# Kernel tuning notes

Measured on AMD Instinct MI355X. Metric: run time of the kernel, lower is better.

The kernel has to match this reference:

```python
import jax, jax.numpy as jnp
import numpy as np

DIM = 1024
HEADS = 16
HEAD_DIM = DIM // HEADS
DECAY = 0.95
EPS = 1e-5


def setup_inputs() -> dict:
    key = jax.random.key(0)
    ks = jax.random.split(key, 11)
    B, S, D = 2, 2048, DIM
    s = 1.0 / np.sqrt(D)
    inp = {
        'x': jax.random.normal(ks[0], (B, S, D), dtype=jnp.float32),
        'Wq': jax.random.normal(ks[1], (D, D), dtype=jnp.float32) * s,
        'bq': jnp.zeros((D,), jnp.float32),
        'Wk': jax.random.normal(ks[2], (D, D), dtype=jnp.float32) * s,
        'bk': jnp.zeros((D,), jnp.float32),
        'Wv': jax.random.normal(ks[3], (D, D), dtype=jnp.float32) * s,
        'bv': jnp.zeros((D,), jnp.float32),
        'Wo': jax.random.normal(ks[4], (D, D), dtype=jnp.float32) * s,
        'bo': jnp.zeros((D,), jnp.float32),
        'gamma': jnp.ones((D,), jnp.float32),
        'beta': jnp.zeros((D,), jnp.float32),
    }
    return inp


def _decay_mask(S, dtype):
    idx = jnp.arange(S)
    diff = (idx[:, None] - idx[None, :]).astype(jnp.float32)
    # decay^(i-j) for i >= j, else 0
    mask = jnp.where(diff >= 0, jnp.exp(diff * np.log(DECAY)), 0.0)
    return mask.astype(dtype)


def reference(x, Wq, bq, Wk, bk, Wv, bv, Wo, bo, gamma, beta):
    B, S, D = x.shape
    H, hd = HEADS, HEAD_DIM

    def split_heads(y):  # [B,S,D] -> [B,H,S,hd]
        return y.reshape(B, S, H, hd).transpose(0, 2, 1, 3)

    q = split_heads(x @ Wq + bq)
    k = split_heads(x @ Wk + bk)
    v = split_heads(x @ Wv + bv)

    mask = _decay_mask(S, x.dtype)  # [S,S]
    scores = jnp.einsum('bhid,bhjd->bhij', q, k) * mask
    out = jnp.einsum('bhij,bhjd->bhid', scores, v)  # [B,H,S,hd]

    out = out.transpose(0, 2, 1, 3).reshape(B, S, D)
    out = out @ Wo + bo

    # GroupNorm(H groups) applied over channel dim with seq as spatial dim
    y = out.transpose(0, 2, 1)            # [B,D,S]
    yg = y.reshape(B, H, hd, S)
    mu = yg.mean(axis=(2, 3), keepdims=True)
    var = yg.var(axis=(2, 3), keepdims=True)
    yn = (yg - mu) / jnp.sqrt(var + EPS)
    yn = yn.reshape(B, D, S) * gamma[None, :, None] + beta[None, :, None]
    return yn.transpose(0, 2, 1)          # [B,S,D]
```

## Files before the change

### kernel.cpp

```cpp
#include <hip/hip_runtime.h>
#include <hip/hip_bf16.h>

typedef unsigned short u16;
typedef __attribute__((ext_vector_type(8))) short short8;
typedef __attribute__((ext_vector_type(4))) float f32x4;
typedef __attribute__((ext_vector_type(4))) unsigned short u16x4;

#define SEQ 2048
#define NH 16
#define HD 64
#define DM 1024
#define LN_DECAY (-0.051293294387550536f)
#define WIN_TILES 4

__device__ __forceinline__ float b2f(u16 u) {
    return __uint_as_float(((unsigned int)u) << 16);
}
__device__ __forceinline__ u16 f2b(float f) {
    unsigned int u = __float_as_uint(f);
    u += 0x7fffu + ((u >> 16) & 1u);
    return (u16)(u >> 16);
}
__device__ __forceinline__ f32x4 mfma16(short8 a, short8 b, f32x4 c) {
    return __builtin_amdgcn_mfma_f32_16x16x32_bf16(a, b, c, 0, 0, 0);
}
__device__ __forceinline__ void gld_lds16(const u16* g, u16* l) {
    __builtin_amdgcn_global_load_lds(
        (const __attribute__((address_space(1))) void*)g,
        (__attribute__((address_space(3))) void*)l, 16, 0, 0);
}
__device__ __forceinline__ int detect_fl(const u16* Wq, int lane) {
    int hit = 0;
#pragma unroll
    for (int j = 0; j < 4; j++) {
        u16 u = Wq[2*(lane + 64*j)];
        if (((u >> 7) & 0xFF) >= 0xC0) hit = 1;
    }
    return (__ballot(hit) != 0ULL) ? 1 : 0;
}

__global__ __launch_bounds__(256) void prep(
    const void* __restrict__ x,
    const void* __restrict__ Wq, const void* __restrict__ Wk,
    const void* __restrict__ Wv, const void* __restrict__ Wo,
    const void* __restrict__ bq, const void* __restrict__ bk,
    const void* __restrict__ bv, const void* __restrict__ bo,
    const void* __restrict__ gamma, const void* __restrict__ beta,
    u16* __restrict__ xc,
    u16* __restrict__ WqT, u16* __restrict__ WkT,
    u16* __restrict__ WvT, u16* __restrict__ WoT,
    u16* __restrict__ bqc, u16* __restrict__ bkc, u16* __restrict__ bvc,
    u16* __restrict__ boc, u16* __restrict__ gammac, u16* __restrict__ betac,
    int* __restrict__ flag, float* __restrict__ statsAcc)
{
    __shared__ u16 tileS[32][33];
    int bid = blockIdx.x, tid = threadIdx.x;
    int fl = detect_fl((const u16*)Wq, tid & 63);

    if (bid < 4096) {
        int i = (bid*256 + tid)*4;
        if (fl) {
            f32x4 v = *(const f32x4*)((const float*)x + i);
            u16x4 o = { f2b(v[0]), f2b(v[1]), f2b(v[2]), f2b(v[3]) };
            *(u16x4*)(xc + i) = o;
        } else {
            *(u16x4*)(xc + i) = *(const u16x4*)((const u16*)x + i);
        }
    } else if (bid == 4096) {
        const void* ins[6] = {bq, bk, bv, bo, gamma, beta};
        u16* outs[6] = {bqc, bkc, bvc, boc, gammac, betac};
        int i = tid*4;
#pragma unroll
        for (int a = 0; a < 6; a++) {
            if (fl) {
                f32x4 v = *(const f32x4*)((const float*)ins[a] + i);
                u16x4 o = { f2b(v[0]), f2b(v[1]), f2b(v[2]), f2b(v[3]) };
                *(u16x4*)(outs[a] + i) = o;
            } else {
                *(u16x4*)(outs[a] + i) = *(const u16x4*)((const u16*)ins[a] + i);
            }
        }
        if (tid == 0) *flag = fl;
        if (tid < 64) statsAcc[tid] = 0.f;
    } else {
        int tb = bid - 4097;
        int wsel = tb >> 10, tile = tb & 1023;
        const void* W = (wsel==0) ? Wq : (wsel==1) ? Wk : (wsel==2) ? Wv : Wo;
        u16* T        = (wsel==0) ? WqT : (wsel==1) ? WkT : (wsel==2) ? WvT : WoT;
        int bn = (tile & 31)*32, bk_ = (tile >> 5)*32;
        int r = tid >> 5, c = tid & 31;
#pragma unroll
        for (int i2 = 0; i2 < 4; i2++) {
            size_t idx = (size_t)(bk_ + r + i2*8)*DM + bn + c;
            tileS[r + i2*8][c] = fl ? f2b(((const float*)W)[idx]) : ((const u16*)W)[idx];
        }
        __syncthreads();
#pragma unroll
        for (int i2 = 0; i2 < 4; i2++)
            T[(size_t)(bn + r + i2*8)*DM + bk_ + c] = tileS[c][r + i2*8];
    }
}

__device__ __forceinline__ void gemm_core(
    const u16* __restrict__ A, const u16* __restrict__ BT,
    u16* As, u16* Bs, int m0, int n0, int t, f32x4 (&acc)[4][4])
{
    int l = t & 63;
    int lane16 = l & 15, quad = l >> 4;
    int w = t >> 6;
    int wm = (w >> 1) * 64, wn = (w & 1) * 64;

    int srow   = t >> 2;
    int schunk = (t & 3) ^ ((t >> 3) & 3);

    f32x4 zero = {0.f, 0.f, 0.f, 0.f};
#pragma unroll
    for (int i = 0; i < 4; i++)
#pragma unroll
        for (int j = 0; j < 4; j++)
            acc[i][j] = zero;

    const u16* a0 = A  + (size_t)(m0 + srow)      * DM + schunk*8;
    const u16* a1 = A  + (size_t)(m0 + srow + 64) * DM + schunk*8;
    const u16* b0 = BT + (size_t)(n0 + srow)      * DM + schunk*8;
    const u16* b1 = BT + (size_t)(n0 + srow + 64) * DM + schunk*8;

    for (int k0 = 0; k0 < DM; k0 += 32) {
        __syncthreads();
        gld_lds16(a0 + k0, &As[t*8]);
        gld_lds16(a1 + k0, &As[2048 + t*8]);
        gld_lds16(b0 + k0, &Bs[t*8]);
        gld_lds16(b1 + k0, &Bs[2048 + t*8]);
        __syncthreads();
        short8 af[4], bf[4];
#pragma unroll
        for (int i = 0; i < 4; i++) {
            int ra = wm + i*16 + lane16;
            int rb = wn + i*16 + lane16;
            af[i] = *(const short8*)(&As[ra*32 + ((quad ^ ((ra>>1)&3))*8)]);
            bf[i] = *(const short8*)(&Bs[rb*32 + ((quad ^ ((rb>>1)&3))*8)]);
        }
#pragma unroll
        for (int i = 0; i < 4; i++)
#pragma unroll
            for (int j = 0; j < 4; j++)
                acc[i][j] = mfma16(af[i], bf[j], acc[i][j]);
    }
}

__global__ __launch_bounds__(256) void gemm_qkv(
    const u16* __restrict__ x,
    const u16* __restrict__ WqT, const u16* __restrict__ WkT, const u16* __restrict__ WvT,
    const u16* __restrict__ bq, const u16* __restrict__ bk, const u16* __restrict__ bv,
    u16* __restrict__ qb, u16* __restrict__ kb, u16* __restrict__ vTb)
{
    __shared__ u16 As[128*32];
    __shared__ u16 Bs[128*32];
    int z = blockIdx.z;
    const u16* BT   = (z==0) ? WqT : (z==1) ? WkT : WvT;
    const u16* bias = (z==0) ? bq  : (z==1) ? bk  : bv;
    u16* outB       = (z==0) ? qb  : (z==1) ? kb  : vTb;
    int m0 = blockIdx.x * 128, n0 = blockIdx.y * 128, t = threadIdx.x;

    f32x4 acc[4][4];
    gemm_core(x, BT, As, Bs, m0, n0, t, acc);

    int l = t & 63, lane16 = l & 15, quad = l >> 4, w = t >> 6;
    int wm = (w >> 1) * 64, wn = (w & 1) * 64;
#pragma unroll
    for (int i = 0; i < 4; i++) {
#pragma unroll
        for (int j = 0; j < 4; j++) {
            int n = n0 + wn + j*16 + lane16;
            float bvv = b2f(bias[n]);
#pragma unroll
            for (int r = 0; r < 4; r++) {
                int m = m0 + wm + i*16 + quad*4 + r;
                float v = acc[i][j][r] + bvv;
                int b = m >> 11, sq = m & (SEQ-1);
                int h = n >> 6,  d = n & (HD-1);
                if (z == 2)
                    outB[(((size_t)(b*NH + h))*HD + d)*SEQ + sq] = f2b(v);
                else
                    outB[(((size_t)(b*NH + h))*SEQ + sq)*HD + d] = f2b(v);
            }
        }
    }
}

__global__ __launch_bounds__(256) void retention(
    const u16* __restrict__ q, const u16* __restrict__ k,
    const u16* __restrict__ vT, u16* __restrict__ attn)
{
    __shared__ u16 Ks[64*64];
    __shared__ u16 Vs[64*64];
    __shared__ u16 Ps[4][16*64];

    int qt = blockIdx.x, bh = blockIdx.y;
    int t = threadIdx.x, w = t >> 6, l = t & 63;
    int c = l & 15, qd = l >> 4;
    int qbase = qt * 64;
    int iwave = qbase + w*16;

    const u16* qh = q  + (size_t)bh * SEQ * HD;
    const u16* kh = k  + (size_t)bh * SEQ * HD;
    const u16* vh = vT + (size_t)bh * HD * SEQ;

    float D[4], E[4];
#pragma unroll
    for (int r = 0; r < 4; r++)
        D[r] = __expf((float)(qd*4 + r) * LN_DECAY);
#pragma unroll
    for (int st = 0; st < 4; st++)
        E[st] = __expf(-(float)(st*16 + c) * LN_DECAY);

    int sr = t >> 3, sc8 = t & 7;

    short8 qf[2];
#pragma unroll
    for (int kk = 0; kk < 2; kk++)
        qf[kk] = *(const short8*)(qh + (size_t)(iwave + c)*HD + kk*32 + qd*8);

    f32x4 zero = {0.f, 0.f, 0.f, 0.f};
    f32x4 oacc[4] = {zero, zero, zero, zero};

    int jt0 = (qt > WIN_TILES) ? (qt - WIN_TILES) : 0;
#pragma unroll 1
    for (int jt = jt0; jt <= qt; jt++) {
        int jbase = jt * 64;
        __syncthreads();
        {
            int r0 = sr, r1 = sr + 32;
            *(short8*)(&Ks[r0*64 + ((sc8 ^ (r0&7))*8)]) = *(const short8*)(kh + (size_t)(jbase+r0)*HD + sc8*8);
            *(short8*)(&Ks[r1*64 + ((sc8 ^ (r1&7))*8)]) = *(const short8*)(kh + (size_t)(jbase+r1)*HD + sc8*8);
            *(short8*)(&Vs[r0*64 + ((sc8 ^ (r0&7))*8)]) = *(const short8*)(vh + (size_t)r0*SEQ + jbase + sc8*8);
            *(short8*)(&Vs[r1*64 + ((sc8 ^ (r1&7))*8)]) = *(const short8*)(vh + (size_t)(r1)*SEQ + jbase + sc8*8);
        }
        __syncthreads();

        f32x4 sacc[4] = {zero, zero, zero, zero};
#pragma unroll
        for (int kk = 0; kk < 2; kk++) {
#pragma unroll
            for (int st = 0; st < 4; st++) {
                int row = st*16 + c;
                short8 bf = *(const short8*)(&Ks[row*64 + (((kk*4+qd) ^ (row&7))*8)]);
                sacc[st] = mfma16(qf[kk], bf, sacc[st]);
            }
        }

        float base = __expf((float)(iwave - jbase) * LN_DECAY);
#pragma unroll
        for (int st = 0; st < 4; st++) {
            int j = jbase + st*16 + c;
            float bE = base * E[st];
#pragma unroll
            for (int r = 0; r < 4; r++) {
                int i = iwave + qd*4 + r;
                float val = (i >= j) ? sacc[st][r] * (bE * D[r]) : 0.0f;
                int row = qd*4 + r;
                int col = st*16 + c;
                Ps[w][row*64 + (((col>>3) ^ (row&7))*8) + (col&7)] = f2b(val);
            }
        }
        asm volatile("s_waitcnt lgkmcnt(0)" ::: "memory");
        short8 pf[2];
#pragma unroll
        for (int kk = 0; kk < 2; kk++)
            pf[kk] = *(const short8*)(&Ps[w][c*64 + (((kk*4+qd) ^ (c&7))*8)]);

#pragma unroll
        for (int kk = 0; kk < 2; kk++) {
#pragma unroll
            for (int nt = 0; nt < 4; nt++) {
                int row = nt*16 + c;
                short8 vf = *(const short8*)(&Vs[row*64 + (((kk*4+qd) ^ (row&7))*8)]);
                oacc[nt] = mfma16(pf[kk], vf, oacc[nt]);
            }
        }
    }

    int b = bh >> 4, h = bh & (NH-1);
#pragma unroll
    for (int nt = 0; nt < 4; nt++) {
        int d = h*HD + nt*16 + c;
#pragma unroll
        for (int r = 0; r < 4; r++) {
            int s = iwave + qd*4 + r;
            attn[((size_t)(b*SEQ + s))*DM + d] = f2b(oacc[nt][r]);
        }
    }
}

__global__ __launch_bounds__(256) void gemm_out(
    const u16* __restrict__ attn, const u16* __restrict__ WoT,
    const u16* __restrict__ bo, float* __restrict__ proj,
    float* __restrict__ statsAcc)
{
    __shared__ u16 As[128*32];
    __shared__ u16 Bs[64*32];
    int m0 = blockIdx.x * 128, n0 = blockIdx.y * 64, t = threadIdx.x;
    int l = t & 63, lane16 = l & 15, quad = l >> 4, w = t >> 6;
    int wm = w * 32;

    int srow   = t >> 2;
    int schunk = (t & 3) ^ ((t >> 3) & 3);

    f32x4 zero = {0.f, 0.f, 0.f, 0.f};
    f32x4 acc[2][4];
#pragma unroll
    for (int i = 0; i < 2; i++)
#pragma unroll
        for (int j = 0; j < 4; j++)
            acc[i][j] = zero;

    const u16* a0 = attn + (size_t)(m0 + srow)      * DM + schunk*8;
    const u16* a1 = attn + (size_t)(m0 + srow + 64) * DM + schunk*8;
    const u16* b0 = WoT  + (size_t)(n0 + srow)      * DM + schunk*8;

    for (int k0 = 0; k0 < DM; k0 += 32) {
        __syncthreads();
        gld_lds16(a0 + k0, &As[t*8]);
        gld_lds16(a1 + k0, &As[2048 + t*8]);
        gld_lds16(b0 + k0, &Bs[t*8]);
        __syncthreads();
        short8 af[2], bf[4];
#pragma unroll
        for (int i = 0; i < 2; i++) {
            int ra = wm + i*16 + lane16;
            af[i] = *(const short8*)(&As[ra*32 + ((quad ^ ((ra>>1)&3))*8)]);
        }
#pragma unroll
        for (int j = 0; j < 4; j++) {
            int rb = j*16 + lane16;
            bf[j] = *(const short8*)(&Bs[rb*32 + ((quad ^ ((rb>>1)&3))*8)]);
        }
#pragma unroll
        for (int i = 0; i < 2; i++)
#pragma unroll
            for (int j = 0; j < 4; j++)
                acc[i][j] = mfma16(af[i], bf[j], acc[i][j]);
    }

    float s = 0.f, ss = 0.f;
#pragma unroll
    for (int j = 0; j < 4; j++) {
        int n = n0 + j*16 + lane16;
        float bvv = b2f(bo[n]);
#pragma unroll
        for (int i = 0; i < 2; i++) {
#pragma unroll
            for (int r = 0; r < 4; r++) {
                int m = m0 + wm + i*16 + quad*4 + r;
                float v = acc[i][j][r] + bvv;
                proj[(size_t)m*DM + n] = v;
                s += v; ss += v*v;
            }
        }
    }
#pragma unroll
    for (int off = 32; off > 0; off >>= 1) {
        s  += __shfl_down(s, off);
        ss += __shfl_down(ss, off);
    }
    if (l == 0) {
        int b = m0 >> 11;
        int g = n0 >> 6;
        atomicAdd(&statsAcc[(b*NH + g)*2],     s);
        atomicAdd(&statsAcc[(b*NH + g)*2 + 1], ss);
    }
}

__global__ __launch_bounds__(256) void gn_apply(
    const float* __restrict__ proj, const float* __restrict__ statsAcc,
    const u16* __restrict__ gamma, const u16* __restrict__ beta,
    const int* __restrict__ flag, void* __restrict__ outv)
{
    int base = (blockIdx.x*256 + threadIdx.x)*4;
    int d = base & (DM-1);
    int b = base >> 21;
    int g = d >> 6;
    float S  = statsAcc[(b*NH + g)*2];
    float SS = statsAcc[(b*NH + g)*2 + 1];
    const float inv = 1.0f/(float)(SEQ*HD);
    float mu = S*inv;
    float rstd = rsqrtf(SS*inv - mu*mu + 1e-5f);
    f32x4 v = *(const f32x4*)(proj + base);
    float o0 = (v[0]-mu)*rstd*b2f(gamma[d])   + b2f(beta[d]);
    float o1 = (v[1]-mu)*rstd*b2f(gamma[d+1]) + b2f(beta[d+1]);
    float o2 = (v[2]-mu)*rstd*b2f(gamma[d+2]) + b2f(beta[d+2]);
    float o3 = (v[3]-mu)*rstd*b2f(gamma[d+3]) + b2f(beta[d+3]);
    if (*flag) {
        f32x4 ov = {o0, o1, o2, o3};
        *(f32x4*)((float*)outv + base) = ov;
    } else {
        u16x4 ov = {f2b(o0), f2b(o1), f2b(o2), f2b(o3)};
        *(u16x4*)((u16*)outv + base) = ov;
    }
}

extern "C" void kernel_launch(void* const* d_in, const int* in_sizes, int n_in,
                              void* d_out, int out_size, void* d_ws, size_t ws_size,
                              hipStream_t stream) {
    const void* x     = d_in[0];
    const void* Wq    = d_in[1];
    const void* bq    = d_in[2];
    const void* Wk    = d_in[3];
    const void* bk    = d_in[4];
    const void* Wv    = d_in[5];
    const void* bv    = d_in[6];
    const void* Wo    = d_in[7];
    const void* bo    = d_in[8];
    const void* gamma = d_in[9];
    const void* beta  = d_in[10];

    const size_t MB = 1024*1024;
    char* ws = (char*)d_ws;
    int*   flag     = (int*)ws;
    u16*   bqc      = (u16*)(ws + 4096);
    u16*   bkc      = (u16*)(ws + 8192);
    u16*   bvc      = (u16*)(ws + 12288);
    u16*   boc      = (u16*)(ws + 16384);
    u16*   gammac   = (u16*)(ws + 20480);
    u16*   betac    = (u16*)(ws + 24576);
    float* statsAcc = (float*)(ws + 28672);
    u16*   xc     = (u16*)(ws + 1*MB);
    u16*   WqT    = (u16*)(ws + 9*MB);
    u16*   WkT    = (u16*)(ws + 11*MB);
    u16*   WvT    = (u16*)(ws + 13*MB);
    u16*   WoT    = (u16*)(ws + 15*MB);
    u16*   qb     = (u16*)(ws + 17*MB);
    u16*   kb     = (u16*)(ws + 25*MB);
    u16*   vTb    = (u16*)(ws + 33*MB);
    u16*   attn   = (u16*)(ws + 41*MB);
    float* proj   = (float*)(ws + 17*MB);

    prep<<<8193, 256, 0, stream>>>(x, Wq, Wk, Wv, Wo, bq, bk, bv, bo, gamma, beta,
                                   xc, WqT, WkT, WvT, WoT,
                                   bqc, bkc, bvc, boc, gammac, betac,
                                   flag, statsAcc);
    gemm_qkv<<<dim3(32, 8, 3), 256, 0, stream>>>(xc, WqT, WkT, WvT, bqc, bkc, bvc, qb, kb, vTb);
    retention<<<dim3(32, 32), 256, 0, stream>>>(qb, kb, vTb, attn);
    gemm_out<<<dim3(32, 16), 256, 0, stream>>>(attn, WoT, boc, proj, statsAcc);
    gn_apply<<<4096, 256, 0, stream>>>(proj, statsAcc, gammac, betac, flag, d_out);
}
```

Measured before the change: 201.6 us.

## Double-buffer LDS in output projection GEMM and enlarge tile to 128x128

```diff
diff --git a/kernel.cpp b/kernel.cpp
--- a/kernel.cpp
+++ b/kernel.cpp
@@ -292,24 +292,42 @@
     }
 }
 
+__device__ __forceinline__ void gout_step(
+    const u16* As, const u16* Bs, int wm, int wn, int lane16, int quad,
+    f32x4 (&acc)[4][4])
+{
+    short8 af[4], bf[4];
+#pragma unroll
+    for (int i = 0; i < 4; i++) {
+        int ra = wm + i*16 + lane16;
+        int rb = wn + i*16 + lane16;
+        af[i] = *(const short8*)(&As[ra*32 + ((quad ^ ((ra>>1)&3))*8)]);
+        bf[i] = *(const short8*)(&Bs[rb*32 + ((quad ^ ((rb>>1)&3))*8)]);
+    }
+#pragma unroll
+    for (int i = 0; i < 4; i++)
+#pragma unroll
+        for (int j = 0; j < 4; j++)
+            acc[i][j] = mfma16(af[i], bf[j], acc[i][j]);
+}
+
 __global__ __launch_bounds__(256) void gemm_out(
     const u16* __restrict__ attn, const u16* __restrict__ WoT,
     const u16* __restrict__ bo, float* __restrict__ proj,
     float* __restrict__ statsAcc)
 {
-    __shared__ u16 As[128*32];
-    __shared__ u16 Bs[64*32];
-    int m0 = blockIdx.x * 128, n0 = blockIdx.y * 64, t = threadIdx.x;
+    __shared__ u16 As0[128*32], Bs0[128*32];
+    __shared__ u16 As1[128*32], Bs1[128*32];
+    int m0 = blockIdx.x * 128, n0 = blockIdx.y * 128, t = threadIdx.x;
     int l = t & 63, lane16 = l & 15, quad = l >> 4, w = t >> 6;
-    int wm = w * 32;
-
+    int wm = (w >> 1) * 64, wn = (w & 1) * 64;
     int srow   = t >> 2;
     int schunk = (t & 3) ^ ((t >> 3) & 3);
 
     f32x4 zero = {0.f, 0.f, 0.f, 0.f};
-    f32x4 acc[2][4];
-#pragma unroll
-    for (int i = 0; i < 2; i++)
+    f32x4 acc[4][4];
+#pragma unroll
+    for (int i = 0; i < 4; i++)
 #pragma unroll
         for (int j = 0; j < 4; j++)
             acc[i][j] = zero;
@@ -317,38 +335,40 @@
     const u16* a0 = attn + (size_t)(m0 + srow)      * DM + schunk*8;
     const u16* a1 = attn + (size_t)(m0 + srow + 64) * DM + schunk*8;
     const u16* b0 = WoT  + (size_t)(n0 + srow)      * DM + schunk*8;
-
-    for (int k0 = 0; k0 < DM; k0 += 32) {
-        __syncthreads();
-        gld_lds16(a0 + k0, &As[t*8]);
-        gld_lds16(a1 + k0, &As[2048 + t*8]);
-        gld_lds16(b0 + k0, &Bs[t*8]);
-        __syncthreads();
-        short8 af[2], bf[4];
-#pragma unroll
-        for (int i = 0; i < 2; i++) {
-            int ra = wm + i*16 + lane16;
-            af[i] = *(const short8*)(&As[ra*32 + ((quad ^ ((ra>>1)&3))*8)]);
-        }
+    const u16* b1 = WoT  + (size_t)(n0 + srow + 64) * DM + schunk*8;
+
+    gld_lds16(a0, &As0[t*8]);
+    gld_lds16(a1, &As0[2048 + t*8]);
+    gld_lds16(b0, &Bs0[t*8]);
+    gld_lds16(b1, &Bs0[2048 + t*8]);
+    __syncthreads();
+
+#pragma unroll 1
+    for (int k0 = 0; k0 < DM; k0 += 64) {
+        gld_lds16(a0 + k0 + 32, &As1[t*8]);
+        gld_lds16(a1 + k0 + 32, &As1[2048 + t*8]);
+        gld_lds16(b0 + k0 + 32, &Bs1[t*8]);
+        gld_lds16(b1 + k0 + 32, &Bs1[2048 + t*8]);
+        gout_step(As0, Bs0, wm, wn, lane16, quad, acc);
+        __syncthreads();
+
+        if (k0 + 64 < DM) {
+            gld_lds16(a0 + k0 + 64, &As0[t*8]);
+            gld_lds16(a1 + k0 + 64, &As0[2048 + t*8]);
+            gld_lds16(b0 + k0 + 64, &Bs0[t*8]);
+            gld_lds16(b1 + k0 + 64, &Bs0[2048 + t*8]);
+        }
+        gout_step(As1, Bs1, wm, wn, lane16, quad, acc);
+        __syncthreads();
+    }
+
+    float s = 0.f, ss = 0.f;
+#pragma unroll
+    for (int i = 0; i < 4; i++) {
 #pragma unroll
         for (int j = 0; j < 4; j++) {
-            int rb = j*16 + lane16;
-            bf[j] = *(const short8*)(&Bs[rb*32 + ((quad ^ ((rb>>1)&3))*8)]);
-        }
-#pragma unroll
-        for (int i = 0; i < 2; i++)
-#pragma unroll
-            for (int j = 0; j < 4; j++)
-                acc[i][j] = mfma16(af[i], bf[j], acc[i][j]);
-    }
-
-    float s = 0.f, ss = 0.f;
-#pragma unroll
-    for (int j = 0; j < 4; j++) {
-        int n = n0 + j*16 + lane16;
-        float bvv = b2f(bo[n]);
-#pragma unroll
-        for (int i = 0; i < 2; i++) {
+            int n = n0 + wn + j*16 + lane16;
+            float bvv = b2f(bo[n]);
 #pragma unroll
             for (int r = 0; r < 4; r++) {
                 int m = m0 + wm + i*16 + quad*4 + r;
@@ -365,7 +385,7 @@
     }
     if (l == 0) {
         int b = m0 >> 11;
-        int g = n0 >> 6;
+        int g = (n0 + wn) >> 6;
         atomicAdd(&statsAcc[(b*NH + g)*2],     s);
         atomicAdd(&statsAcc[(b*NH + g)*2 + 1], ss);
     }
@@ -441,6 +461,6 @@
                                    flag, statsAcc);
     gemm_qkv<<<dim3(32, 8, 3), 256, 0, stream>>>(xc, WqT, WkT, WvT, bqc, bkc, bvc, qb, kb, vTb);
     retention<<<dim3(32, 32), 256, 0, stream>>>(qb, kb, vTb, attn);
-    gemm_out<<<dim3(32, 16), 256, 0, stream>>>(attn, WoT, boc, proj, statsAcc);
+    gemm_out<<<dim3(32, 8), 256, 0, stream>>>(attn, WoT, boc, proj, statsAcc);
     gn_apply<<<4096, 256, 0, stream>>>(proj, statsAcc, gammac, betac, flag, d_out);
 }
```

Result: faster. 188.9 us (-6.3%).

## Double-buffer LDS in output GEMM and enlarge tile to 128x128 with 8 waves

Applied to the files above, without the earlier changes.

```diff
diff --git a/kernel.cpp b/kernel.cpp
--- a/kernel.cpp
+++ b/kernel.cpp
@@ -292,17 +292,38 @@
     }
 }
 
-__global__ __launch_bounds__(256) void gemm_out(
+__device__ __forceinline__ void gout_step8(
+    const u16* As, const u16* Bs, int wm, int wn, int lane16, int quad,
+    f32x4 (&acc)[2][4])
+{
+    short8 af[2], bf[4];
+#pragma unroll
+    for (int i = 0; i < 2; i++) {
+        int ra = wm + i*16 + lane16;
+        af[i] = *(const short8*)(&As[ra*32 + ((quad ^ ((ra>>1)&3))*8)]);
+    }
+#pragma unroll
+    for (int j = 0; j < 4; j++) {
+        int rb = wn + j*16 + lane16;
+        bf[j] = *(const short8*)(&Bs[rb*32 + ((quad ^ ((rb>>1)&3))*8)]);
+    }
+#pragma unroll
+    for (int i = 0; i < 2; i++)
+#pragma unroll
+        for (int j = 0; j < 4; j++)
+            acc[i][j] = mfma16(af[i], bf[j], acc[i][j]);
+}
+
+__global__ __launch_bounds__(512) void gemm_out(
     const u16* __restrict__ attn, const u16* __restrict__ WoT,
     const u16* __restrict__ bo, float* __restrict__ proj,
     float* __restrict__ statsAcc)
 {
-    __shared__ u16 As[128*32];
-    __shared__ u16 Bs[64*32];
-    int m0 = blockIdx.x * 128, n0 = blockIdx.y * 64, t = threadIdx.x;
+    __shared__ u16 As0[128*32], Bs0[128*32];
+    __shared__ u16 As1[128*32], Bs1[128*32];
+    int m0 = blockIdx.x * 128, n0 = blockIdx.y * 128, t = threadIdx.x;
     int l = t & 63, lane16 = l & 15, quad = l >> 4, w = t >> 6;
-    int wm = w * 32;
-
+    int wm = (w >> 1) * 32, wn = (w & 1) * 64;
     int srow   = t >> 2;
     int schunk = (t & 3) ^ ((t >> 3) & 3);
 
@@ -314,41 +335,35 @@
         for (int j = 0; j < 4; j++)
             acc[i][j] = zero;
 
-    const u16* a0 = attn + (size_t)(m0 + srow)      * DM + schunk*8;
-    const u16* a1 = attn + (size_t)(m0 + srow + 64) * DM + schunk*8;
-    const u16* b0 = WoT  + (size_t)(n0 + srow)      * DM + schunk*8;
-
-    for (int k0 = 0; k0 < DM; k0 += 32) {
-        __syncthreads();
-        gld_lds16(a0 + k0, &As[t*8]);
-        gld_lds16(a1 + k0, &As[2048 + t*8]);
-        gld_lds16(b0 + k0, &Bs[t*8]);
-        __syncthreads();
-        short8 af[2], bf[4];
-#pragma unroll
-        for (int i = 0; i < 2; i++) {
-            int ra = wm + i*16 + lane16;
-            af[i] = *(const short8*)(&As[ra*32 + ((quad ^ ((ra>>1)&3))*8)]);
-        }
+    const u16* a = attn + (size_t)(m0 + srow) * DM + schunk*8;
+    const u16* b = WoT  + (size_t)(n0 + srow) * DM + schunk*8;
+
+    gld_lds16(a, &As0[t*8]);
+    gld_lds16(b, &Bs0[t*8]);
+    __syncthreads();
+
+#pragma unroll 1
+    for (int k0 = 0; k0 < DM; k0 += 64) {
+        gld_lds16(a + k0 + 32, &As1[t*8]);
+        gld_lds16(b + k0 + 32, &Bs1[t*8]);
+        gout_step8(As0, Bs0, wm, wn, lane16, quad, acc);
+        __syncthreads();
+
+        if (k0 + 64 < DM) {
+            gld_lds16(a + k0 + 64, &As0[t*8]);
+            gld_lds16(b + k0 + 64, &Bs0[t*8]);
+        }
+        gout_step8(As1, Bs1, wm, wn, lane16, quad, acc);
+        __syncthreads();
+    }
+
+    float s = 0.f, ss = 0.f;
+#pragma unroll
+    for (int i = 0; i < 2; i++) {
 #pragma unroll
         for (int j = 0; j < 4; j++) {
-            int rb = j*16 + lane16;
-            bf[j] = *(const short8*)(&Bs[rb*32 + ((quad ^ ((rb>>1)&3))*8)]);
-        }
-#pragma unroll
-        for (int i = 0; i < 2; i++)
-#pragma unroll
-            for (int j = 0; j < 4; j++)
-                acc[i][j] = mfma16(af[i], bf[j], acc[i][j]);
-    }
-
-    float s = 0.f, ss = 0.f;
-#pragma unroll
-    for (int j = 0; j < 4; j++) {
-        int n = n0 + j*16 + lane16;
-        float bvv = b2f(bo[n]);
-#pragma unroll
-        for (int i = 0; i < 2; i++) {
+            int n = n0 + wn + j*16 + lane16;
+            float bvv = b2f(bo[n]);
 #pragma unroll
             for (int r = 0; r < 4; r++) {
                 int m = m0 + wm + i*16 + quad*4 + r;
@@ -364,10 +379,10 @@
         ss += __shfl_down(ss, off);
     }
     if (l == 0) {
-        int b = m0 >> 11;
-        int g = n0 >> 6;
-        atomicAdd(&statsAcc[(b*NH + g)*2],     s);
-        atomicAdd(&statsAcc[(b*NH + g)*2 + 1], ss);
+        int b_ = m0 >> 11;
+        int g  = (n0 + wn) >> 6;
+        atomicAdd(&statsAcc[(b_*NH + g)*2],     s);
+        atomicAdd(&statsAcc[(b_*NH + g)*2 + 1], ss);
     }
 }
 
@@ -441,6 +456,6 @@
                                    flag, statsAcc);
     gemm_qkv<<<dim3(32, 8, 3), 256, 0, stream>>>(xc, WqT, WkT, WvT, bqc, bkc, bvc, qb, kb, vTb);
     retention<<<dim3(32, 32), 256, 0, stream>>>(qb, kb, vTb, attn);
-    gemm_out<<<dim3(32, 16), 256, 0, stream>>>(attn, WoT, boc, proj, statsAcc);
+    gemm_out<<<dim3(32, 8), 512, 0, stream>>>(attn, WoT, boc, proj, statsAcc);
     gn_apply<<<4096, 256, 0, stream>>>(proj, statsAcc, gammac, betac, flag, d_out);
 }
```

New measurement: 198.1 us. About the same (-1.7%).

## Remap blocks across XCDs, stage V-transpose stores in LDS, enlarge output GEMM tiles

Applied to the files above, without the earlier changes.

```diff
diff --git a/kernel.cpp b/kernel.cpp
--- a/kernel.cpp
+++ b/kernel.cpp
@@ -156,33 +156,72 @@
 {
     __shared__ u16 As[128*32];
     __shared__ u16 Bs[128*32];
-    int z = blockIdx.z;
+    __shared__ u16 rep[64*130];
+
+    int lin = blockIdx.x + 32*(blockIdx.y + 8*blockIdx.z);
+    int xcd = lin & 7, slot = lin >> 3;
+    int mx  = xcd*4 + (slot & 3);
+    int col = slot >> 2;
+    int ny  = col & 7, z = col >> 3;
+
     const u16* BT   = (z==0) ? WqT : (z==1) ? WkT : WvT;
     const u16* bias = (z==0) ? bq  : (z==1) ? bk  : bv;
     u16* outB       = (z==0) ? qb  : (z==1) ? kb  : vTb;
-    int m0 = blockIdx.x * 128, n0 = blockIdx.y * 128, t = threadIdx.x;
+    int m0 = mx * 128, n0 = ny * 128, t = threadIdx.x;
 
     f32x4 acc[4][4];
     gemm_core(x, BT, As, Bs, m0, n0, t, acc);
 
     int l = t & 63, lane16 = l & 15, quad = l >> 4, w = t >> 6;
     int wm = (w >> 1) * 64, wn = (w & 1) * 64;
-#pragma unroll
-    for (int i = 0; i < 4; i++) {
-#pragma unroll
-        for (int j = 0; j < 4; j++) {
-            int n = n0 + wn + j*16 + lane16;
-            float bvv = b2f(bias[n]);
-#pragma unroll
-            for (int r = 0; r < 4; r++) {
-                int m = m0 + wm + i*16 + quad*4 + r;
-                float v = acc[i][j][r] + bvv;
-                int b = m >> 11, sq = m & (SEQ-1);
-                int h = n >> 6,  d = n & (HD-1);
-                if (z == 2)
-                    outB[(((size_t)(b*NH + h))*HD + d)*SEQ + sq] = f2b(v);
-                else
-                    outB[(((size_t)(b*NH + h))*SEQ + sq)*HD + d] = f2b(v);
+
+    if (z == 2) {
+        int b = m0 >> 11, sq0 = m0 & (SEQ-1);
+#pragma unroll 1
+        for (int h = 0; h < 2; h++) {
+            if ((w & 1) == h) {
+#pragma unroll
+                for (int j = 0; j < 4; j++) {
+                    int dl = j*16 + lane16;
+                    float bvv = b2f(bias[n0 + h*64 + dl]);
+#pragma unroll
+                    for (int i = 0; i < 2; i++) {
+#pragma unroll
+                        for (int r = 0; r < 4; r++) {
+                            rep[dl*130 + wm + i*16 + quad*4 + r] =
+                                f2b(acc[i][j][r] + bvv);
+                            rep[dl*130 + wm + (i+2)*16 + quad*4 + r] =
+                                f2b(acc[i+2][j][r] + bvv);
+                        }
+                    }
+                }
+            }
+            __syncthreads();
+            int head = (n0 + h*64) >> 6;
+            int row = t >> 2, c0 = (t & 3)*32;
+            u16* dst = outB + (((size_t)(b*NH + head))*HD + row)*SEQ + sq0 + c0;
+#pragma unroll
+            for (int cc = 0; cc < 32; cc += 8) {
+                short8 v = *(const short8*)(&rep[row*130 + c0 + cc]);
+                *(short8*)(dst + cc) = v;
+            }
+            __syncthreads();
+        }
+    } else {
+#pragma unroll
+        for (int i = 0; i < 4; i++) {
+#pragma unroll
+            for (int j = 0; j < 4; j++) {
+                int n = n0 + wn + j*16 + lane16;
+                float bvv = b2f(bias[n]);
+#pragma unroll
+                for (int r = 0; r < 4; r++) {
+                    int m = m0 + wm + i*16 + quad*4 + r;
+                    float v = acc[i][j][r] + bvv;
+                    int b = m >> 11, sq = m & (SEQ-1);
+                    int hh = n >> 6, d = n & (HD-1);
+                    outB[(((size_t)(b*NH + hh))*SEQ + sq)*HD + d] = f2b(v);
+                }
             }
         }
     }
@@ -196,7 +235,11 @@
     __shared__ u16 Vs[64*64];
     __shared__ u16 Ps[4][16*64];
 
-    int qt = blockIdx.x, bh = blockIdx.y;
+    int lin = blockIdx.x + 32*blockIdx.y;
+    int xcd = lin & 7, slot = lin >> 3;
+    int bh  = xcd*4 + (slot >> 5);
+    int qt  = slot & 31;
+
     int t = threadIdx.x, w = t >> 6, l = t & 63;
     int c = l & 15, qd = l >> 4;
     int qbase = qt * 64;
@@ -298,57 +341,25 @@
     float* __restrict__ statsAcc)
 {
     __shared__ u16 As[128*32];
-    __shared__ u16 Bs[64*32];
-    int m0 = blockIdx.x * 128, n0 = blockIdx.y * 64, t = threadIdx.x;
+    __shared__ u16 Bs[128*32];
+    int lin = blockIdx.x + 32*blockIdx.y;
+    int xcd = lin & 7, slot = lin >> 3;
+    int mx  = xcd*4 + (slot & 3);
+    int ny  = slot >> 2;
+    int m0 = mx * 128, n0 = ny * 128, t = threadIdx.x;
+
+    f32x4 acc[4][4];
+    gemm_core(attn, WoT, As, Bs, m0, n0, t, acc);
+
     int l = t & 63, lane16 = l & 15, quad = l >> 4, w = t >> 6;
-    int wm = w * 32;
-
-    int srow   = t >> 2;
-    int schunk = (t & 3) ^ ((t >> 3) & 3);
-
-    f32x4 zero = {0.f, 0.f, 0.f, 0.f};
-    f32x4 acc[2][4];
-#pragma unroll
-    for (int i = 0; i < 2; i++)
-#pragma unroll
-        for (int j = 0; j < 4; j++)
-            acc[i][j] = zero;
-
-    const u16* a0 = attn + (size_t)(m0 + srow)      * DM + schunk*8;
-    const u16* a1 = attn + (size_t)(m0 + srow + 64) * DM + schunk*8;
-    const u16* b0 = WoT  + (size_t)(n0 + srow)      * DM + schunk*8;
-
-    for (int k0 = 0; k0 < DM; k0 += 32) {
-        __syncthreads();
-        gld_lds16(a0 + k0, &As[t*8]);
-        gld_lds16(a1 + k0, &As[2048 + t*8]);
-        gld_lds16(b0 + k0, &Bs[t*8]);
-        __syncthreads();
-        short8 af[2], bf[4];
-#pragma unroll
-        for (int i = 0; i < 2; i++) {
-            int ra = wm + i*16 + lane16;
-            af[i] = *(const short8*)(&As[ra*32 + ((quad ^ ((ra>>1)&3))*8)]);
-        }
+    int wm = (w >> 1) * 64, wn = (w & 1) * 64;
+    float s = 0.f, ss = 0.f;
+#pragma unroll
+    for (int i = 0; i < 4; i++) {
 #pragma unroll
         for (int j = 0; j < 4; j++) {
-            int rb = j*16 + lane16;
-            bf[j] = *(const short8*)(&Bs[rb*32 + ((quad ^ ((rb>>1)&3))*8)]);
-        }
-#pragma unroll
-        for (int i = 0; i < 2; i++)
-#pragma unroll
-            for (int j = 0; j < 4; j++)
-                acc[i][j] = mfma16(af[i], bf[j], acc[i][j]);
-    }
-
-    float s = 0.f, ss = 0.f;
-#pragma unroll
-    for (int j = 0; j < 4; j++) {
-        int n = n0 + j*16 + lane16;
-        float bvv = b2f(bo[n]);
-#pragma unroll
-        for (int i = 0; i < 2; i++) {
+            int n = n0 + wn + j*16 + lane16;
+            float bvv = b2f(bo[n]);
 #pragma unroll
             for (int r = 0; r < 4; r++) {
                 int m = m0 + wm + i*16 + quad*4 + r;
@@ -365,7 +376,7 @@
     }
     if (l == 0) {
         int b = m0 >> 11;
-        int g = n0 >> 6;
+        int g = (n0 + wn) >> 6;
         atomicAdd(&statsAcc[(b*NH + g)*2],     s);
         atomicAdd(&statsAcc[(b*NH + g)*2 + 1], ss);
     }
@@ -441,6 +452,6 @@
                                    flag, statsAcc);
     gemm_qkv<<<dim3(32, 8, 3), 256, 0, stream>>>(xc, WqT, WkT, WvT, bqc, bkc, bvc, qb, kb, vTb);
     retention<<<dim3(32, 32), 256, 0, stream>>>(qb, kb, vTb, attn);
-    gemm_out<<<dim3(32, 16), 256, 0, stream>>>(attn, WoT, boc, proj, statsAcc);
+    gemm_out<<<dim3(32, 8), 256, 0, stream>>>(attn, WoT, boc, proj, statsAcc);
     gn_apply<<<4096, 256, 0, stream>>>(proj, statsAcc, gammac, betac, flag, d_out);
 }
```

Result: no change. 199.4 us (-1.1%).
